# Kernel tuning notes

Hardware: AMD Instinct MI355X
Metric: run time of the kernel (lower is better)

Reference implementation:

```python
import jax, jax.numpy as jnp
import numpy as np

B, T, D, S, L, V, C = 32, 2048, 512, 64, 4, 32000, 2
EPS = 1e-5

def layernorm(x, w, b):
    m = jnp.mean(x, axis=-1, keepdims=True)
    v = jnp.var(x, axis=-1, keepdims=True)
    return (x - m) / jnp.sqrt(v + EPS) * w + b

def setup_inputs() -> dict:
    key = jax.random.key(0)
    ks = jax.random.split(key, 10)
    std = 0.02
    def n(k, shape, s=std):
        return jax.random.normal(k, shape, dtype=jnp.float32) * s
    return {
        "tokens": jax.random.randint(ks[0], (B, T), 0, V),
        "emb": n(ks[1], (V, D)),
        "ln_w": jnp.ones((L, D), jnp.float32), "ln_b": jnp.zeros((L, D), jnp.float32),
        "Wsp": n(ks[2], (L, S, D)), "bsp": jnp.zeros((L, S), jnp.float32),
        "Wip": n(ks[3], (L, S, D)), "bip": jnp.zeros((L, S), jnp.float32),
        "Wop": n(ks[4], (L, D, S)), "bop": jnp.zeros((L, D), jnp.float32),
        "Wg": n(ks[5], (L, D, D)), "bg": jnp.zeros((L, D), jnp.float32),
        "A": n(ks[6], (L, S, S), 0.01),  # state_transition
        "fln_w": jnp.ones((D,), jnp.float32), "fln_b": jnp.zeros((D,), jnp.float32),
        "W1": n(ks[7], (D // 2, D)), "b1": jnp.zeros((D // 2,), jnp.float32),
        "W2": n(ks[8], (C, D // 2)), "b2": jnp.zeros((C,), jnp.float32),
    }

def _block(x, ln_w, ln_b, Wsp, bsp, Wip, bip, Wop, bop, Wg, bg, A):
    # x: [B,T,D]
    res = x
    xn = layernorm(x, ln_w, ln_b)
    # precompute input-driven terms for all timesteps (hoisted out of the scan)
    u = (jnp.einsum('btd,sd->bts', xn, Wsp) + bsp
         + jnp.einsum('btd,sd->bts', xn, Wip) + bip)          # [B,T,S]
    g = jax.nn.sigmoid(jnp.einsum('btd,ed->bte', xn, Wg) + bg)  # [B,T,D]
    h0 = jnp.zeros((x.shape[0], A.shape[0]), x.dtype)
    def step(h, u_t):
        h = jnp.tanh(h @ A.T + u_t)
        return h, h
    _, hs = jax.lax.scan(step, h0, jnp.swapaxes(u, 0, 1))  # hs: [T,B,S]
    out = jnp.einsum('tbs,ds->btd', hs, Wop) + bop           # [B,T,D]
    return out * g + res  # dropout is identity in eval

def reference(tokens, emb, ln_w, ln_b, Wsp, bsp, Wip, bip, Wop, bop, Wg, bg, A,
              fln_w, fln_b, W1, b1, W2, b2):
    x = emb[tokens] * jnp.sqrt(jnp.asarray(D, jnp.float32))  # [B,T,D]
    for l in range(L):
        x = _block(x, ln_w[l], ln_b[l], Wsp[l], bsp[l], Wip[l], bip[l],
                   Wop[l], bop[l], Wg[l], bg[l], A[l])
    x = jnp.mean(layernorm(x, fln_w, fln_b), axis=1)  # [B,D]
    h = jax.nn.relu(x @ W1.T + b1)
    return h @ W2.T + b2  # [B,C]
```

## Files before the change

kernel.cpp:

```cpp
#include <hip/hip_runtime.h>


#define DEV __device__ __forceinline__

typedef __attribute__((ext_vector_type(8))) short short8v;
typedef __attribute__((ext_vector_type(4))) float f32x4;

static constexpr int Bn = 32, Tn = 2048, Dn = 512, Sn = 64, Lk = 4;
static constexpr int Mrows = Bn * Tn;

DEV unsigned short f2bf(float f) {
  unsigned u = __float_as_uint(f);
  u += 0x7fffu + ((u >> 16) & 1u);
  return (unsigned short)(u >> 16);
}
DEV float bf2f(unsigned short h) { return __uint_as_float(((unsigned)h) << 16); }

DEV void g2lds16(const void* g, void* l) {
  __builtin_amdgcn_global_load_lds(
      (const __attribute__((address_space(1))) void*)g,
      (__attribute__((address_space(3))) void*)l, 16, 0, 0);
}

template <int THREADS, int ROWS>
DEV void stage_sw(const char* gbase, size_t rowStride, size_t kOff, char* lds, int tid) {
#pragma unroll
  for (int r = 0; r < ROWS * 128 / (THREADS * 16); ++r) {
    int o = r * THREADS * 16 + tid * 16;
    int row = o >> 7, kb = o & 127;
    g2lds16(gbase + (size_t)row * rowStride + kOff + (size_t)(kb ^ ((row & 7) << 4)),
            lds + o);
  }
}

__global__ __launch_bounds__(256) void prep_kernel(
    const float* __restrict__ Wg, const float* __restrict__ Wop,
    const float* __restrict__ Wsp, const float* __restrict__ Wip,
    const float* __restrict__ bsp, const float* __restrict__ bip,
    const float* __restrict__ lnw, const float* __restrict__ lnb,
    unsigned short* __restrict__ WgP, unsigned short* __restrict__ WuP,
    unsigned short* __restrict__ WopB,
    float* __restrict__ P, float* __restrict__ Q,
    float* __restrict__ Pu, float* __restrict__ Qu, float* __restrict__ bu) {
  const int blk = blockIdx.x, tid = threadIdx.x, lane = tid & 63, w = tid >> 6;
  if (blk < 512) {
    int idx = blk * 4 + w;
    int l = idx >> 9;
    const float* src = Wg + (size_t)idx * 512;
    const float* gw = lnw + (size_t)l * 512;
    const float* gb = lnb + (size_t)l * 512;
    unsigned short* dst = WgP + (size_t)idx * 512;
    float p = 0.f, q = 0.f;
#pragma unroll
    for (int e = 0; e < 8; ++e) {
      int k = lane * 8 + e;
      float wv = src[k];
      unsigned short hb = f2bf(gw[k] * wv);
      dst[k] = hb;
      p += bf2f(hb);
      q += gb[k] * wv;
    }
#pragma unroll
    for (int m = 32; m >= 1; m >>= 1) { p += __shfl_xor(p, m); q += __shfl_xor(q, m); }
    if (lane == 0) { P[idx] = p; Q[idx] = q; }
  } else if (blk < 576) {
    int idx = (blk - 512) * 4 + w;
    int l = idx >> 6;
    const float* s1 = Wsp + (size_t)idx * 512;
    const float* s2 = Wip + (size_t)idx * 512;
    const float* gw = lnw + (size_t)l * 512;
    const float* gb = lnb + (size_t)l * 512;
    unsigned short* dst = WuP + (size_t)idx * 512;
    float p = 0.f, q = 0.f;
#pragma unroll
    for (int e = 0; e < 8; ++e) {
      int k = lane * 8 + e;
      float wv = s1[k] + s2[k];
      unsigned short hb = f2bf(gw[k] * wv);
      dst[k] = hb;
      p += bf2f(hb);
      q += gb[k] * wv;
    }
#pragma unroll
    for (int m = 32; m >= 1; m >>= 1) { p += __shfl_xor(p, m); q += __shfl_xor(q, m); }
    if (lane == 0) { Pu[idx] = p; Qu[idx] = q; bu[idx] = bsp[idx] + bip[idx]; }
  } else {
    int i = (blk - 576) * 256 + tid;
    if (i < Lk * Dn * Sn) WopB[i] = f2bf(Wop[i]);
  }
}

template <int EMB>
__global__ __launch_bounds__(256) void ln_u_kernel(
    const unsigned short* __restrict__ x,
    const int* __restrict__ tok,
    const float* __restrict__ emb,
    unsigned short* __restrict__ xw,
    const unsigned short* __restrict__ WuP,
    const float* __restrict__ Pu, const float* __restrict__ Qu,
    const float* __restrict__ bu,
    unsigned short* __restrict__ u,
    float* __restrict__ meanA, float* __restrict__ rstdA) {
  __shared__ __align__(16) unsigned short As[32 * 512];
  __shared__ __align__(16) unsigned short Bs[64 * 256];
  __shared__ float mS[32], rS[32];
  const int tid = threadIdx.x, lane = tid & 63, w = tid >> 6;
  const int row0 = blockIdx.x * 32;

#pragma unroll 2
  for (int i = 0; i < 8; ++i) {
    int row = w * 8 + i;
    size_t grow = (size_t)(row0 + row);
    short8v v;
    if (EMB) {
      int t = tok[grow];
      const float4* src = (const float4*)(emb + (size_t)t * Dn + lane * 8);
      float4 a = src[0], b = src[1];
      const float scale = 22.627416997969522f;
      v[0] = (short)f2bf(a.x * scale); v[1] = (short)f2bf(a.y * scale);
      v[2] = (short)f2bf(a.z * scale); v[3] = (short)f2bf(a.w * scale);
      v[4] = (short)f2bf(b.x * scale); v[5] = (short)f2bf(b.y * scale);
      v[6] = (short)f2bf(b.z * scale); v[7] = (short)f2bf(b.w * scale);
      *(short8v*)(xw + grow * 512 + lane * 8) = v;
    } else {
      v = *(const short8v*)(x + grow * 512 + lane * 8);
    }
    float f0 = bf2f((unsigned short)v[0]), f1 = bf2f((unsigned short)v[1]);
    float f2 = bf2f((unsigned short)v[2]), f3 = bf2f((unsigned short)v[3]);
    float f4 = bf2f((unsigned short)v[4]), f5 = bf2f((unsigned short)v[5]);
    float f6 = bf2f((unsigned short)v[6]), f7 = bf2f((unsigned short)v[7]);
    float s = (f0 + f1) + (f2 + f3) + (f4 + f5) + (f6 + f7);
    float q = f0*f0 + f1*f1 + f2*f2 + f3*f3 + f4*f4 + f5*f5 + f6*f6 + f7*f7;
#pragma unroll
    for (int m = 32; m >= 1; m >>= 1) { s += __shfl_xor(s, m); q += __shfl_xor(q, m); }
    float mean = s * (1.f / 512.f);
    float var  = q * (1.f / 512.f) - mean * mean;
    float rstd = 1.f / sqrtf(var + 1e-5f);
    *(short8v*)&As[row * 512 + ((lane * 8) ^ ((row & 7) << 3))] = v;
    if (lane == 0) { mS[row] = mean; rS[row] = rstd; meanA[grow] = mean; rstdA[grow] = rstd; }
  }
  const char* Wb = (const char*)WuP;
#pragma unroll
  for (int r = 0; r < 8; ++r) {
    int o = r * 4096 + tid * 16;
    int row = o >> 9, kb = o & 511;
    g2lds16(Wb + (size_t)row * 1024 + (size_t)(kb ^ ((row & 7) << 4)), (char*)Bs + o);
  }
  __syncthreads();

  const int wr = w >> 1, wc = w & 1;
  f32x4 acc[2] = {};
  const int rs = lane & 15, kx = (lane >> 4) * 8;
  const int key = (rs & 7) << 3;
  const int arow = (wr * 16 + rs) * 512;
#pragma unroll
  for (int p = 0; p < 2; ++p) {
#pragma unroll
    for (int kt = 0; kt < 8; ++kt) {
      short8v a = *(const short8v*)&As[arow + ((p * 256 + kt * 32 + kx) ^ key)];
#pragma unroll
      for (int n = 0; n < 2; ++n) {
        int col = wc * 32 + n * 16 + rs;
        short8v b = *(const short8v*)&Bs[col * 256 + ((kt * 32 + kx) ^ key)];
        acc[n] = __builtin_amdgcn_mfma_f32_16x16x32_bf16(a, b, acc[n], 0, 0, 0);
      }
    }
    if (p == 0) {
      __syncthreads();
#pragma unroll
      for (int r = 0; r < 8; ++r) {
        int o = r * 4096 + tid * 16;
        int row = o >> 9, kb = o & 511;
        g2lds16(Wb + (size_t)row * 1024 + 512 + (size_t)(kb ^ ((row & 7) << 4)),
                (char*)Bs + o);
      }
      __syncthreads();
    }
  }
  const int ccol = lane & 15, cr4 = (lane >> 4) * 4;
#pragma unroll
  for (int n = 0; n < 2; ++n) {
    int col = wc * 32 + n * 16 + ccol;
    float pc = Pu[col], c1 = Qu[col] + bu[col];
#pragma unroll
    for (int j = 0; j < 4; ++j) {
      int row = wr * 16 + cr4 + j;
      float sr = rS[row], mr = mS[row];
      float val = fmaf(sr, acc[n][j], fmaf(-mr * sr, pc, c1));
      u[(size_t)(row0 + row) * 64 + col] = f2bf(val);
    }
  }
}

__global__ __launch_bounds__(256) void gemm_gateop(
    const unsigned short* __restrict__ x,
    const unsigned short* __restrict__ hs,
    const unsigned short* __restrict__ WgP,
    const unsigned short* __restrict__ WopB,
    const float* __restrict__ P, const float* __restrict__ Q,
    const float* __restrict__ bg, const float* __restrict__ bop,
    const float* __restrict__ meanA, const float* __restrict__ rstdA,
    unsigned short* __restrict__ xout) {
  __shared__ __align__(16) unsigned short As[128 * 64];
  __shared__ __align__(16) unsigned short Bs[128 * 64];
  const int tid = threadIdx.x, lane = tid & 63, wave = tid >> 6;
  const int wr = wave >> 1, wc = wave & 1;
  const int L = blockIdx.x;
  const int xcd = L & 7, rnd = L >> 3;
  const int row0 = ((rnd >> 2) * 8 + xcd) * 128;
  const int col0 = (rnd & 3) * 128;
  f32x4 accg[4][4] = {};
  f32x4 acco[4][4] = {};
  const int rs = lane & 15;
  const int swu = (rs & 7) << 3;

  const char* Ab = (const char*)(x + (size_t)row0 * 512);
  const char* Bb = (const char*)(WgP + (size_t)col0 * 512);
  for (int kt = 0; kt < 512; kt += 64) {
    stage_sw<256, 128>(Ab, 1024, (size_t)kt * 2, (char*)As, tid);
    stage_sw<256, 128>(Bb, 1024, (size_t)kt * 2, (char*)Bs, tid);
    __syncthreads();
#pragma unroll
    for (int kk = 0; kk < 2; ++kk) {
      const int ks = (kk * 32 + (lane >> 4) * 8) ^ swu;
      short8v af[4], bfv[4];
#pragma unroll
      for (int m = 0; m < 4; ++m)
        af[m] = *(const short8v*)&As[(wr * 64 + m * 16 + rs) * 64 + ks];
#pragma unroll
      for (int n = 0; n < 4; ++n)
        bfv[n] = *(const short8v*)&Bs[(wc * 64 + n * 16 + rs) * 64 + ks];
#pragma unroll
      for (int m = 0; m < 4; ++m)
#pragma unroll
        for (int n = 0; n < 4; ++n)
          accg[m][n] = __builtin_amdgcn_mfma_f32_16x16x32_bf16(af[m], bfv[n], accg[m][n], 0, 0, 0);
    }
    __syncthreads();
  }

  stage_sw<256, 128>((const char*)(hs + (size_t)row0 * 64), 128, 0, (char*)As, tid);
  stage_sw<256, 128>((const char*)(WopB + (size_t)col0 * 64), 128, 0, (char*)Bs, tid);
  __syncthreads();
#pragma unroll
  for (int kk = 0; kk < 2; ++kk) {
    const int ks = (kk * 32 + (lane >> 4) * 8) ^ swu;
    short8v af[4], bfv[4];
#pragma unroll
    for (int m = 0; m < 4; ++m)
      af[m] = *(const short8v*)&As[(wr * 64 + m * 16 + rs) * 64 + ks];
#pragma unroll
    for (int n = 0; n < 4; ++n)
      bfv[n] = *(const short8v*)&Bs[(wc * 64 + n * 16 + rs) * 64 + ks];
#pragma unroll
    for (int m = 0; m < 4; ++m)
#pragma unroll
      for (int n = 0; n < 4; ++n)
        acco[m][n] = __builtin_amdgcn_mfma_f32_16x16x32_bf16(af[m], bfv[n], acco[m][n], 0, 0, 0);
  }

  const int ccol = lane & 15, cr4 = (lane >> 4) * 4;
#pragma unroll
  for (int m = 0; m < 4; ++m) {
    float sr4[4], mr4[4];
#pragma unroll
    for (int j = 0; j < 4; ++j) {
      int grow = row0 + wr * 64 + m * 16 + cr4 + j;
      sr4[j] = rstdA[grow];
      mr4[j] = meanA[grow];
    }
#pragma unroll
    for (int n = 0; n < 4; ++n) {
      int gcol = col0 + wc * 64 + n * 16 + ccol;
      float pc = P[gcol], c1 = Q[gcol] + bg[gcol], bov = bop[gcol];
#pragma unroll
      for (int j = 0; j < 4; ++j) {
        int grow = row0 + wr * 64 + m * 16 + cr4 + j;
        size_t idx = (size_t)grow * 512 + gcol;
        float gpre = fmaf(sr4[j], accg[m][n][j], fmaf(-mr4[j] * sr4[j], pc, c1));
        float gv = 1.f / (1.f + __expf(-gpre));
        float ov = acco[m][n][j] + bov;
        xout[idx] = f2bf(bf2f(x[idx]) + gv * ov);
      }
    }
  }
}

__global__ __launch_bounds__(64) void scan_kernel(const unsigned short* __restrict__ u,
                                                  const float* __restrict__ A,
                                                  unsigned short* __restrict__ hs) {
  const int l = threadIdx.x;
  const int b = blockIdx.y, c = blockIdx.x;
  __shared__ float h[Sn];
  h[l] = 0.f;

  float4 Ar[16];
  const float4* Arow = (const float4*)(A + (size_t)l * Sn);
#pragma unroll
  for (int i = 0; i < 16; ++i) Ar[i] = Arow[i];

  int t0 = c * 64 - 16; if (t0 < 0) t0 = 0;
  const int tw = c * 64, tend = c * 64 + 64;
  const unsigned short* ub = u + (size_t)b * Tn * Sn;
  unsigned short* hb = hs + (size_t)b * Tn * Sn;

  unsigned short uraw = ub[(size_t)t0 * Sn + l];
  for (int t = t0; t < tend; ++t) {
    int tnext = t + 1 < Tn ? t + 1 : Tn - 1;
    unsigned short unext = ub[(size_t)tnext * Sn + l];
    const float4* h4 = (const float4*)h;
    float a0 = bf2f(uraw), a1 = 0.f, a2 = 0.f, a3 = 0.f;
#pragma unroll
    for (int i = 0; i < 16; i += 4) {
      float4 h0 = h4[i], h1 = h4[i + 1], h2 = h4[i + 2], h3 = h4[i + 3];
      a0 += Ar[i].x * h0.x + Ar[i].y * h0.y + Ar[i].z * h0.z + Ar[i].w * h0.w;
      a1 += Ar[i+1].x * h1.x + Ar[i+1].y * h1.y + Ar[i+1].z * h1.z + Ar[i+1].w * h1.w;
      a2 += Ar[i+2].x * h2.x + Ar[i+2].y * h2.y + Ar[i+2].z * h2.z + Ar[i+2].w * h2.w;
      a3 += Ar[i+3].x * h3.x + Ar[i+3].y * h3.y + Ar[i+3].z * h3.z + Ar[i+3].w * h3.w;
    }
    float sv = (a0 + a1) + (a2 + a3);
    sv = fminf(fmaxf(sv, -15.f), 15.f);
    float e = __expf(2.f * sv);
    float hn = __fdividef(e - 1.f, e + 1.f);
    if (t >= tw) hb[(size_t)t * Sn + l] = f2bf(hn);
    h[l] = hn;
    uraw = unext;
  }
}

__global__ __launch_bounds__(256) void final_ln_mean(const unsigned short* __restrict__ x,
                                                     const float* __restrict__ fw,
                                                     const float* __restrict__ fb,
                                                     float* __restrict__ part) {
  const int b = blockIdx.y, chunk = blockIdx.x;
  const int wave = threadIdx.x >> 6, lane = threadIdx.x & 63;
  const float4* wp = (const float4*)(fw + lane * 8);
  const float4* bp = (const float4*)(fb + lane * 8);
  float4 w0 = wp[0], w1 = wp[1], bb0 = bp[0], bb1 = bp[1];
  float acc[8] = {};
  for (int it = 0; it < 64; ++it) {
    int t = chunk * 256 + it * 4 + wave;
    short8v v = *(const short8v*)(x + ((size_t)b * Tn + t) * Dn + lane * 8);
    float f0 = bf2f((unsigned short)v[0]), f1 = bf2f((unsigned short)v[1]);
    float f2 = bf2f((unsigned short)v[2]), f3 = bf2f((unsigned short)v[3]);
    float f4 = bf2f((unsigned short)v[4]), f5 = bf2f((unsigned short)v[5]);
    float f6 = bf2f((unsigned short)v[6]), f7 = bf2f((unsigned short)v[7]);
    float s = (f0 + f1) + (f2 + f3) + (f4 + f5) + (f6 + f7);
#pragma unroll
    for (int m = 32; m >= 1; m >>= 1) s += __shfl_xor(s, m);
    float mean = s * (1.f / 512.f);
    float d0 = f0 - mean, d1 = f1 - mean, d2 = f2 - mean, d3 = f3 - mean;
    float d4 = f4 - mean, d5 = f5 - mean, d6 = f6 - mean, d7 = f7 - mean;
    float q = d0*d0 + d1*d1 + d2*d2 + d3*d3 + d4*d4 + d5*d5 + d6*d6 + d7*d7;
#pragma unroll
    for (int m = 32; m >= 1; m >>= 1) q += __shfl_xor(q, m);
    float rstd = 1.f / sqrtf(q * (1.f / 512.f) + 1e-5f);
    acc[0] += d0 * rstd * w0.x + bb0.x;
    acc[1] += d1 * rstd * w0.y + bb0.y;
    acc[2] += d2 * rstd * w0.z + bb0.z;
    acc[3] += d3 * rstd * w0.w + bb0.w;
    acc[4] += d4 * rstd * w1.x + bb1.x;
    acc[5] += d5 * rstd * w1.y + bb1.y;
    acc[6] += d6 * rstd * w1.z + bb1.z;
    acc[7] += d7 * rstd * w1.w + bb1.w;
  }
  __shared__ float red[4][512];
#pragma unroll
  for (int j = 0; j < 8; ++j) red[wave][lane * 8 + j] = acc[j];
  __syncthreads();
#pragma unroll
  for (int cc = 0; cc < 2; ++cc) {
    int cidx = threadIdx.x * 2 + cc;
    part[((size_t)(chunk * Bn + b)) * Dn + cidx] =
        red[0][cidx] + red[1][cidx] + red[2][cidx] + red[3][cidx];
  }
}

__global__ __launch_bounds__(256) void head_kernel(const float* __restrict__ part,
                                                   const float* __restrict__ W1,
                                                   const float* __restrict__ b1,
                                                   const float* __restrict__ W2,
                                                   const float* __restrict__ b2,
                                                   float* __restrict__ out) {
  const int b = blockIdx.x, j = threadIdx.x;
  __shared__ float ybuf[Dn];
  for (int d = j; d < Dn; d += 256) {
    float s = 0.f;
#pragma unroll
    for (int ch = 0; ch < 8; ++ch) s += part[((size_t)(ch * Bn + b)) * Dn + d];
    ybuf[d] = s * (1.f / 2048.f);
  }
  __syncthreads();
  const float4* wj = (const float4*)(W1 + (size_t)j * Dn);
  const float4* yb = (const float4*)ybuf;
  float a0 = 0.f, a1 = 0.f, a2 = 0.f, a3 = 0.f;
  for (int k = 0; k < 128; k += 4) {
    float4 q0 = wj[k], q1 = wj[k+1], q2 = wj[k+2], q3 = wj[k+3];
    float4 u0 = yb[k], u1 = yb[k+1], u2 = yb[k+2], u3 = yb[k+3];
    a0 += q0.x*u0.x + q0.y*u0.y + q0.z*u0.z + q0.w*u0.w;
    a1 += q1.x*u1.x + q1.y*u1.y + q1.z*u1.z + q1.w*u1.w;
    a2 += q2.x*u2.x + q2.y*u2.y + q2.z*u2.z + q2.w*u2.w;
    a3 += q3.x*u3.x + q3.y*u3.y + q3.z*u3.z + q3.w*u3.w;
  }
  float hv = fmaxf((a0 + a1) + (a2 + a3) + b1[j], 0.f);
  __shared__ float red[256];
  for (int c = 0; c < 2; ++c) {
    red[j] = hv * W2[c * 256 + j];
    __syncthreads();
    for (int s2 = 128; s2 > 0; s2 >>= 1) {
      if (j < s2) red[j] += red[j + s2];
      __syncthreads();
    }
    if (j == 0) out[b * 2 + c] = red[0] + b2[c];
    __syncthreads();
  }
}

static constexpr size_t WGP_OFF  = 0;
static constexpr size_t WUP_OFF  = 2097152;
static constexpr size_t WOPB_OFF = 2359296;
static constexpr size_t P_OFF    = 2621440;
static constexpr size_t Q_OFF    = 2629632;
static constexpr size_t PU_OFF   = 2637824;
static constexpr size_t QU_OFF   = 2638848;
static constexpr size_t BU_OFF   = 2639872;
static constexpr size_t PART_OFF = 2640896;
static constexpr size_t X_OFF    = 3165184;
static constexpr size_t X2_OFF   = X_OFF + 67108864;
static constexpr size_t CH_OFF   = X2_OFF + 67108864;

extern "C" void kernel_launch(void* const* d_in, const int* in_sizes, int n_in,
                              void* d_out, int out_size, void* d_ws, size_t ws_size,
                              hipStream_t stream) {
  const int*   tok  = (const int*)d_in[0];
  const float* emb  = (const float*)d_in[1];
  const float* ln_w = (const float*)d_in[2];
  const float* ln_b = (const float*)d_in[3];
  const float* Wsp  = (const float*)d_in[4];
  const float* bsp  = (const float*)d_in[5];
  const float* Wip  = (const float*)d_in[6];
  const float* bip  = (const float*)d_in[7];
  const float* Wop  = (const float*)d_in[8];
  const float* bop  = (const float*)d_in[9];
  const float* Wg   = (const float*)d_in[10];
  const float* bg   = (const float*)d_in[11];
  const float* Am   = (const float*)d_in[12];
  const float* fw   = (const float*)d_in[13];
  const float* fb   = (const float*)d_in[14];
  const float* W1   = (const float*)d_in[15];
  const float* b1   = (const float*)d_in[16];
  const float* W2   = (const float*)d_in[17];
  const float* b2   = (const float*)d_in[18];

  char* ws = (char*)d_ws;
  unsigned short* WgP  = (unsigned short*)(ws + WGP_OFF);
  unsigned short* WuP  = (unsigned short*)(ws + WUP_OFF);
  unsigned short* WopB = (unsigned short*)(ws + WOPB_OFF);
  float* Pg  = (float*)(ws + P_OFF);
  float* Qg  = (float*)(ws + Q_OFF);
  float* Pu  = (float*)(ws + PU_OFF);
  float* Qu  = (float*)(ws + QU_OFF);
  float* bu  = (float*)(ws + BU_OFF);
  float* part= (float*)(ws + PART_OFF);
  unsigned short* xA = (unsigned short*)(ws + X_OFF);
  unsigned short* xB = (unsigned short*)(ws + X2_OFF);
  float* outp = (float*)d_out;

  int nch = 32;
  for (int c = 1; c <= 32; c <<= 1) {
    size_t Mc = (size_t)Mrows / c;
    if (CH_OFF + 264ull * Mc <= ws_size) { nch = c; break; }
  }
  const int nb = Bn / nch;
  const size_t Mc = (size_t)Mrows / nch;
  unsigned short* u    = (unsigned short*)(ws + CH_OFF);
  unsigned short* hs   = (unsigned short*)(ws + CH_OFF + 128ull * Mc);
  float*          mean = (float*)(ws + CH_OFF + 256ull * Mc);
  float*          rstd = (float*)(ws + CH_OFF + 260ull * Mc);

  prep_kernel<<<1088, 256, 0, stream>>>(Wg, Wop, Wsp, Wip, bsp, bip, ln_w, ln_b,
                                        WgP, WuP, WopB, Pg, Qg, Pu, Qu, bu);

  for (int l = 0; l < Lk; ++l) {
    unsigned short* src = (l & 1) ? xB : xA;
    unsigned short* dst = (l & 1) ? xA : xB;
    for (int c = 0; c < nch; ++c) {
      unsigned short* xs = src + (size_t)c * Mc * Dn;
      unsigned short* xd = dst + (size_t)c * Mc * Dn;
      if (l == 0)
        ln_u_kernel<1><<<(int)(Mc / 32), 256, 0, stream>>>(
            nullptr, tok + (size_t)c * Mc, emb, xs,
            WuP + (size_t)l * Sn * Dn, Pu + l * Sn, Qu + l * Sn, bu + l * Sn,
            u, mean, rstd);
      else
        ln_u_kernel<0><<<(int)(Mc / 32), 256, 0, stream>>>(
            xs, nullptr, nullptr, nullptr,
            WuP + (size_t)l * Sn * Dn, Pu + l * Sn, Qu + l * Sn, bu + l * Sn,
            u, mean, rstd);
      scan_kernel<<<dim3(Tn / 64, nb), 64, 0, stream>>>(
          u, Am + (size_t)l * Sn * Sn, hs);
      gemm_gateop<<<(int)(Mc / 128) * 4, 256, 0, stream>>>(
          xs, hs, WgP + (size_t)l * Dn * Dn, WopB + (size_t)l * Dn * Sn,
          Pg + l * Dn, Qg + l * Dn, bg + l * Dn, bop + l * Dn,
          mean, rstd, xd);
    }
  }

  final_ln_mean<<<dim3(8, Bn), 256, 0, stream>>>(xA, fw, fb, part);
  head_kernel<<<Bn, 256, 0, stream>>>(part, W1, b1, W2, b2, outp);
}
```

Baseline: 735.0 us.

## Double-buffer gate GEMM LDS tiles and async-load LN input to LDS

The gate/output GEMM kernel now uses two LDS buffers per operand, so the next K-tile (and finally the hs/Wop tile) is prefetched while MFMAs run on the current one, which removes one barrier per iteration. In the LN+u kernel, the non-embedding path loads the x rows straight into swizzled LDS with global_load_lds and issues the weight loads at the same time, so the LN statistics are computed from LDS after one barrier. Doubling LDS in the GEMM kernel (to 64KB) may lower occupancy.

```diff
diff --git a/kernel.cpp b/kernel.cpp
--- a/kernel.cpp
+++ b/kernel.cpp
@@ -106,25 +106,48 @@
   __shared__ float mS[32], rS[32];
   const int tid = threadIdx.x, lane = tid & 63, w = tid >> 6;
   const int row0 = blockIdx.x * 32;
-
+  const char* Wb = (const char*)WuP;
+
+  if (EMB) {
 #pragma unroll 2
-  for (int i = 0; i < 8; ++i) {
-    int row = w * 8 + i;
-    size_t grow = (size_t)(row0 + row);
-    short8v v;
-    if (EMB) {
+    for (int i = 0; i < 8; ++i) {
+      int row = w * 8 + i;
+      size_t grow = (size_t)(row0 + row);
       int t = tok[grow];
       const float4* src = (const float4*)(emb + (size_t)t * Dn + lane * 8);
       float4 a = src[0], b = src[1];
       const float scale = 22.627416997969522f;
+      short8v v;
       v[0] = (short)f2bf(a.x * scale); v[1] = (short)f2bf(a.y * scale);
       v[2] = (short)f2bf(a.z * scale); v[3] = (short)f2bf(a.w * scale);
       v[4] = (short)f2bf(b.x * scale); v[5] = (short)f2bf(b.y * scale);
       v[6] = (short)f2bf(b.z * scale); v[7] = (short)f2bf(b.w * scale);
       *(short8v*)(xw + grow * 512 + lane * 8) = v;
-    } else {
-      v = *(const short8v*)(x + grow * 512 + lane * 8);
-    }
+      *(short8v*)&As[row * 512 + ((lane * 8) ^ ((row & 7) << 3))] = v;
+    }
+  } else {
+    const char* Xb = (const char*)(x + (size_t)row0 * 512);
+#pragma unroll
+    for (int r = 0; r < 8; ++r) {
+      int o = r * 4096 + tid * 16;
+      int row = o >> 10, kb = o & 1023;
+      g2lds16(Xb + (size_t)row * 1024 + (size_t)(kb ^ ((row & 7) << 4)),
+              (char*)As + o);
+    }
+  }
+#pragma unroll
+  for (int r = 0; r < 8; ++r) {
+    int o = r * 4096 + tid * 16;
+    int row = o >> 9, kb = o & 511;
+    g2lds16(Wb + (size_t)row * 1024 + (size_t)(kb ^ ((row & 7) << 4)), (char*)Bs + o);
+  }
+  __syncthreads();
+
+#pragma unroll 2
+  for (int i = 0; i < 8; ++i) {
+    int row = w * 8 + i;
+    size_t grow = (size_t)(row0 + row);
+    short8v v = *(const short8v*)&As[row * 512 + ((lane * 8) ^ ((row & 7) << 3))];
     float f0 = bf2f((unsigned short)v[0]), f1 = bf2f((unsigned short)v[1]);
     float f2 = bf2f((unsigned short)v[2]), f3 = bf2f((unsigned short)v[3]);
     float f4 = bf2f((unsigned short)v[4]), f5 = bf2f((unsigned short)v[5]);
@@ -136,17 +159,8 @@
     float mean = s * (1.f / 512.f);
     float var  = q * (1.f / 512.f) - mean * mean;
     float rstd = 1.f / sqrtf(var + 1e-5f);
-    *(short8v*)&As[row * 512 + ((lane * 8) ^ ((row & 7) << 3))] = v;
     if (lane == 0) { mS[row] = mean; rS[row] = rstd; meanA[grow] = mean; rstdA[grow] = rstd; }
   }
-  const char* Wb = (const char*)WuP;
-#pragma unroll
-  for (int r = 0; r < 8; ++r) {
-    int o = r * 4096 + tid * 16;
-    int row = o >> 9, kb = o & 511;
-    g2lds16(Wb + (size_t)row * 1024 + (size_t)(kb ^ ((row & 7) << 4)), (char*)Bs + o);
-  }
-  __syncthreads();
 
   const int wr = w >> 1, wc = w & 1;
   f32x4 acc[2] = {};
@@ -201,8 +215,8 @@
     const float* __restrict__ bg, const float* __restrict__ bop,
     const float* __restrict__ meanA, const float* __restrict__ rstdA,
     unsigned short* __restrict__ xout) {
-  __shared__ __align__(16) unsigned short As[128 * 64];
-  __shared__ __align__(16) unsigned short Bs[128 * 64];
+  __shared__ __align__(16) unsigned short As[2][128 * 64];
+  __shared__ __align__(16) unsigned short Bs[2][128 * 64];
   const int tid = threadIdx.x, lane = tid & 63, wave = tid >> 6;
   const int wr = wave >> 1, wc = wave & 1;
   const int L = blockIdx.x;
@@ -216,20 +230,32 @@
 
   const char* Ab = (const char*)(x + (size_t)row0 * 512);
   const char* Bb = (const char*)(WgP + (size_t)col0 * 512);
-  for (int kt = 0; kt < 512; kt += 64) {
-    stage_sw<256, 128>(Ab, 1024, (size_t)kt * 2, (char*)As, tid);
-    stage_sw<256, 128>(Bb, 1024, (size_t)kt * 2, (char*)Bs, tid);
-    __syncthreads();
+
+  stage_sw<256, 128>(Ab, 1024, 0, (char*)As[0], tid);
+  stage_sw<256, 128>(Bb, 1024, 0, (char*)Bs[0], tid);
+  __syncthreads();
+
+  int cur = 0;
+  for (int kt = 0; kt < 8; ++kt) {
+    if (kt < 7) {
+      stage_sw<256, 128>(Ab, 1024, (size_t)(kt + 1) * 128, (char*)As[cur ^ 1], tid);
+      stage_sw<256, 128>(Bb, 1024, (size_t)(kt + 1) * 128, (char*)Bs[cur ^ 1], tid);
+    } else {
+      stage_sw<256, 128>((const char*)(hs + (size_t)row0 * 64), 128, 0,
+                         (char*)As[cur ^ 1], tid);
+      stage_sw<256, 128>((const char*)(WopB + (size_t)col0 * 64), 128, 0,
+                         (char*)Bs[cur ^ 1], tid);
+    }
 #pragma unroll
     for (int kk = 0; kk < 2; ++kk) {
       const int ks = (kk * 32 + (lane >> 4) * 8) ^ swu;
       short8v af[4], bfv[4];
 #pragma unroll
       for (int m = 0; m < 4; ++m)
-        af[m] = *(const short8v*)&As[(wr * 64 + m * 16 + rs) * 64 + ks];
+        af[m] = *(const short8v*)&As[cur][(wr * 64 + m * 16 + rs) * 64 + ks];
 #pragma unroll
       for (int n = 0; n < 4; ++n)
-        bfv[n] = *(const short8v*)&Bs[(wc * 64 + n * 16 + rs) * 64 + ks];
+        bfv[n] = *(const short8v*)&Bs[cur][(wc * 64 + n * 16 + rs) * 64 + ks];
 #pragma unroll
       for (int m = 0; m < 4; ++m)
 #pragma unroll
@@ -237,21 +263,19 @@
           accg[m][n] = __builtin_amdgcn_mfma_f32_16x16x32_bf16(af[m], bfv[n], accg[m][n], 0, 0, 0);
     }
     __syncthreads();
-  }
-
-  stage_sw<256, 128>((const char*)(hs + (size_t)row0 * 64), 128, 0, (char*)As, tid);
-  stage_sw<256, 128>((const char*)(WopB + (size_t)col0 * 64), 128, 0, (char*)Bs, tid);
-  __syncthreads();
+    cur ^= 1;
+  }
+
 #pragma unroll
   for (int kk = 0; kk < 2; ++kk) {
     const int ks = (kk * 32 + (lane >> 4) * 8) ^ swu;
     short8v af[4], bfv[4];
 #pragma unroll
     for (int m = 0; m < 4; ++m)
-      af[m] = *(const short8v*)&As[(wr * 64 + m * 16 + rs) * 64 + ks];
+      af[m] = *(const short8v*)&As[cur][(wr * 64 + m * 16 + rs) * 64 + ks];
 #pragma unroll
     for (int n = 0; n < 4; ++n)
-      bfv[n] = *(const short8v*)&Bs[(wc * 64 + n * 16 + rs) * 64 + ks];
+      bfv[n] = *(const short8v*)&Bs[cur][(wc * 64 + n * 16 + rs) * 64 + ks];
 #pragma unroll
     for (int m = 0; m < 4; ++m)
 #pragma unroll
```

Result: slower. 880.9 us (+19.8%).
